# Kernel tuning notes

Hardware: AMD Instinct MI355X
Metric: run time of the kernel (lower is better)

## Reference

```python
import jax, jax.numpy as jnp
import numpy as np

BZ, MCN, HS, NC, LED, NT = 256, 128, 768, 7, 128, 2
EPS = 1e-12


def setup_inputs():
    key = jax.random.key(0)
    ks = jax.random.split(key, 16)
    def n(k, shape, sc=0.02):
        return jax.random.normal(k, shape, jnp.float32) * sc
    G4 = 4 * HS
    return {
        'clause_vector': jax.random.normal(ks[0], (BZ, MCN, HS), jnp.float32),
        'clause_num_mask': jnp.ones((BZ, MCN), jnp.float32),
        'target_labels': jax.random.uniform(ks[1], (BZ, MCN, NC), jnp.float32),
        'label_embed': n(ks[2], (NC, LED)),
        'Wq': n(ks[3], (HS, HS)), 'bq': jnp.zeros((HS,), jnp.float32),
        'Wk': n(ks[4], (HS, HS)), 'bk': jnp.zeros((HS,), jnp.float32),
        'Wv': n(ks[5], (HS, HS)), 'bv': jnp.zeros((HS,), jnp.float32),
        'Wo': n(ks[6], (HS, HS)), 'bo': jnp.zeros((HS,), jnp.float32),
        'ln_g': jnp.ones((HS,), jnp.float32), 'ln_b': jnp.zeros((HS,), jnp.float32),
        'Wp': n(ks[7], (HS, LED + 2 * HS)), 'bp': jnp.zeros((HS,), jnp.float32),
        'W_ih0': n(ks[8], (G4, HS)), 'W_hh0': n(ks[9], (G4, HS)),
        'b_ih0': jnp.zeros((G4,), jnp.float32), 'b_hh0': jnp.zeros((G4,), jnp.float32),
        'W_ih1': n(ks[10], (G4, HS)), 'W_hh1': n(ks[11], (G4, HS)),
        'b_ih1': jnp.zeros((G4,), jnp.float32), 'b_hh1': jnp.zeros((G4,), jnp.float32),
        'Wout': n(ks[12], (NC, HS)), 'bout': jnp.zeros((NC,), jnp.float32),
    }


def _layer_norm(x, g, b):
    mu = jnp.mean(x, -1, keepdims=True)
    var = jnp.mean(jnp.square(x - mu), -1, keepdims=True)
    return (x - mu) / jnp.sqrt(var + EPS) * g + b


def _forward(clause_vector, clause_num_mask, target_labels, label_embed,
             Wq, bq, Wk, bk, Wv, bv, Wo, bo, ln_g, ln_b, Wp, bp,
             W_ih0, W_hh0, b_ih0, b_hh0, W_ih1, W_hh1, b_ih1, b_hh1, Wout, bout):
    bz, mcn, hs = clause_vector.shape
    nc = Wout.shape[0]
    scale = float(1.0 / np.sqrt(hs))  # single head => head_size == hs
    # K/V depend only on clause_vector: hoist out of the decode loop
    K = clause_vector @ Wk.T + bk  # [bz, mcn, hs]
    V = clause_vector @ Wv.T + bv  # [bz, mcn, hs]
    mask_add = (1.0 - clause_num_mask) * -10000.0  # [bz, mcn]
    # step-0 labels: zeros with neutral (last) class set to 1 (remain_neutral)
    init_label = jnp.zeros((bz, nc), clause_vector.dtype).at[:, -1].set(1.0)
    # teacher forcing: step t>0 uses target_labels[:, t-1]
    lp_seq = jnp.concatenate([init_label[None], jnp.swapaxes(target_labels, 0, 1)[:-1]], 0)  # [mcn,bz,nc]
    cv_seq = jnp.swapaxes(clause_vector, 0, 1)  # [mcn, bz, hs]
    layers = ((W_ih0, W_hh0, b_ih0, b_hh0), (W_ih1, W_hh1, b_ih1, b_hh1))

    def step(carry, xs):
        h_all, c_all = carry  # [NT, bz, hs] each
        cv_t, lp = xs
        h = h_all[-1]  # decoder_hidden (dropout is identity in eval)
        emb = lp @ label_embed  # bmm(last_pred, label_embed) -> [bz, led]
        q = h @ Wq.T + bq
        scores = jnp.einsum('bh,bmh->bm', q, K) * scale + mask_add
        probs = jax.nn.softmax(scores, -1)
        ctx = jnp.einsum('bm,bmh->bh', probs, V)
        # BertSelfOutput: LayerNorm(dense(ctx) + residual)
        attn = _layer_norm(ctx @ Wo.T + bo + h, ln_g, ln_b)
        x = jnp.concatenate([emb, attn, cv_t], -1) @ Wp.T + bp  # [bz, hs]
        hs_new, cs_new = [], []
        for l, (Wih, Whh, bih, bhh) in enumerate(layers):
            gates = x @ Wih.T + bih + h_all[l] @ Whh.T + bhh  # [bz, 4hs]
            i, f, g, o = jnp.split(gates, 4, -1)  # torch gate order i,f,g,o
            c = jax.nn.sigmoid(f) * c_all[l] + jax.nn.sigmoid(i) * jnp.tanh(g)
            x = jax.nn.sigmoid(o) * jnp.tanh(c)
            hs_new.append(x)
            cs_new.append(c)
        h_all = jnp.stack(hs_new)
        c_all = jnp.stack(cs_new)
        pred = h_all[-1] @ Wout.T + bout  # raw logits (teacher-forcing branch)
        return (h_all, c_all), pred

    zeros = jnp.zeros((NT, bz, hs), clause_vector.dtype)
    _, preds = jax.lax.scan(step, (zeros, zeros), (cv_seq, lp_seq))
    return jnp.swapaxes(preds, 0, 1)  # [bz, mcn, nc]


def reference(clause_vector, clause_num_mask, target_labels, label_embed,
              Wq, bq, Wk, bk, Wv, bv, Wo, bo, ln_g, ln_b, Wp, bp,
              W_ih0, W_hh0, b_ih0, b_hh0, W_ih1, W_hh1, b_ih1, b_hh1, Wout, bout):
    return _forward(clause_vector, clause_num_mask, target_labels, label_embed,
                    Wq, bq, Wk, bk, Wv, bv, Wo, bo, ln_g, ln_b, Wp, bp,
                    W_ih0, W_hh0, b_ih0, b_hh0, W_ih1, W_hh1, b_ih1, b_hh1, Wout, bout)
```

## Files before the change

kernel.cpp:

```cpp
#include <hip/hip_runtime.h>
#include <hip/hip_bf16.h>
#include <math.h>

#define BZ 256
#define MCN 128
#define HS 768
#define NC 7
#define LED 128
#define G4 3072
#define LDP (LED + 2 * HS)

#define TBM 64
#define TBN 64
#define TBK 16

__device__ __forceinline__ ushort f2bf(float f) {
    uint x = __float_as_uint(f);
    uint r = (x + 0x7fffu + ((x >> 16) & 1u)) >> 16;
    return (ushort)r;
}
__device__ __forceinline__ float bf2f(ushort u) {
    return __uint_as_float(((uint)u) << 16);
}

__global__ __launch_bounds__(256) void gemm_abt(
    const float* __restrict__ A, int lda,
    const float* __restrict__ B, int ldb,
    const float* __restrict__ bias,
    const float* __restrict__ add, long add_ld,
    float* __restrict__ C, ushort* __restrict__ Cbf, int ldc, int K)
{
    __shared__ float As[TBK][TBM + 4];
    __shared__ float Bs[TBK][TBN + 4];
    const int tid = threadIdx.x;
    const int m0 = blockIdx.y * TBM;
    const int n0 = blockIdx.x * TBN;
    const int tx = tid & 15, ty = tid >> 4;
    const int lrow = tid >> 2;
    const int lcol = (tid & 3) * 4;
    float acc[4][4] = {};
    const float* Ap = A + (size_t)(m0 + lrow) * lda + lcol;
    const float* Bp = B + (size_t)(n0 + lrow) * ldb + lcol;
    for (int k0 = 0; k0 < K; k0 += TBK) {
        float4 av = *(const float4*)(Ap + k0);
        float4 bv = *(const float4*)(Bp + k0);
        As[lcol + 0][lrow] = av.x; As[lcol + 1][lrow] = av.y;
        As[lcol + 2][lrow] = av.z; As[lcol + 3][lrow] = av.w;
        Bs[lcol + 0][lrow] = bv.x; Bs[lcol + 1][lrow] = bv.y;
        Bs[lcol + 2][lrow] = bv.z; Bs[lcol + 3][lrow] = bv.w;
        __syncthreads();
        #pragma unroll
        for (int kk = 0; kk < TBK; ++kk) {
            float4 a4 = *(const float4*)&As[kk][ty * 4];
            float4 b4 = *(const float4*)&Bs[kk][tx * 4];
            float a[4] = {a4.x, a4.y, a4.z, a4.w};
            float b[4] = {b4.x, b4.y, b4.z, b4.w};
            #pragma unroll
            for (int i = 0; i < 4; ++i)
                #pragma unroll
                for (int j = 0; j < 4; ++j)
                    acc[i][j] += a[i] * b[j];
        }
        __syncthreads();
    }
    #pragma unroll
    for (int i = 0; i < 4; ++i) {
        int m = m0 + ty * 4 + i;
        #pragma unroll
        for (int j = 0; j < 4; ++j) {
            float v = acc[i][j];
            if (bias) v += bias[n0 + tx * 4 + j];
            if (add)  v += add[(size_t)m * add_ld + n0 + tx * 4 + j];
            if (Cbf) Cbf[(size_t)m * ldc + n0 + tx * 4 + j] = f2bf(v);
            else     C  [(size_t)m * ldc + n0 + tx * 4 + j] = v;
        }
    }
}

__global__ __launch_bounds__(256) void gemm_ab(
    const float* __restrict__ A, int lda,
    const float* __restrict__ B, int ldb,
    float* __restrict__ C, int ldc, int K)
{
    __shared__ float As[TBK][TBM + 4];
    __shared__ float Bs[TBK][TBN + 4];
    const int tid = threadIdx.x;
    const int m0 = blockIdx.y * TBM, n0 = blockIdx.x * TBN;
    const int tx = tid & 15, ty = tid >> 4;
    float acc[4][4] = {};
    for (int k0 = 0; k0 < K; k0 += TBK) {
        #pragma unroll
        for (int i = 0; i < 4; ++i) {
            int idx = tid + i * 256;
            int r = idx >> 4, kk = idx & 15;
            As[kk][r] = A[(size_t)(m0 + r) * lda + k0 + kk];
        }
        #pragma unroll
        for (int i = 0; i < 4; ++i) {
            int idx = tid + i * 256;
            int kk = idx >> 6, cc = idx & 63;
            Bs[kk][cc] = B[(size_t)(k0 + kk) * ldb + n0 + cc];
        }
        __syncthreads();
        #pragma unroll
        for (int kk = 0; kk < TBK; ++kk) {
            float4 a4 = *(const float4*)&As[kk][ty * 4];
            float4 b4 = *(const float4*)&Bs[kk][tx * 4];
            float a[4] = {a4.x, a4.y, a4.z, a4.w};
            float b[4] = {b4.x, b4.y, b4.z, b4.w};
            #pragma unroll
            for (int i = 0; i < 4; ++i)
                #pragma unroll
                for (int j = 0; j < 4; ++j)
                    acc[i][j] += a[i] * b[j];
        }
        __syncthreads();
    }
    #pragma unroll
    for (int i = 0; i < 4; ++i) {
        float* Cr = C + (size_t)(m0 + ty * 4 + i) * ldc + n0 + tx * 4;
        #pragma unroll
        for (int j = 0; j < 4; ++j) Cr[j] = acc[i][j];
    }
}

__global__ __launch_bounds__(256) void gemm_atb(
    const float* __restrict__ A, int lda,
    const float* __restrict__ B, int ldb,
    float* __restrict__ C, int ldc, int K, float alpha)
{
    __shared__ float As[TBK][TBM + 4];
    __shared__ float Bs[TBK][TBN + 4];
    const int tid = threadIdx.x;
    const int m0 = blockIdx.y * TBM, n0 = blockIdx.x * TBN;
    const int tx = tid & 15, ty = tid >> 4;
    float acc[4][4] = {};
    for (int k0 = 0; k0 < K; k0 += TBK) {
        #pragma unroll
        for (int i = 0; i < 4; ++i) {
            int idx = tid + i * 256;
            int kk = idx >> 6, r = idx & 63;
            As[kk][r] = A[(size_t)(k0 + kk) * lda + m0 + r];
            Bs[kk][r] = B[(size_t)(k0 + kk) * ldb + n0 + r];
        }
        __syncthreads();
        #pragma unroll
        for (int kk = 0; kk < TBK; ++kk) {
            float4 a4 = *(const float4*)&As[kk][ty * 4];
            float4 b4 = *(const float4*)&Bs[kk][tx * 4];
            float a[4] = {a4.x, a4.y, a4.z, a4.w};
            float b[4] = {b4.x, b4.y, b4.z, b4.w};
            #pragma unroll
            for (int i = 0; i < 4; ++i)
                #pragma unroll
                for (int j = 0; j < 4; ++j)
                    acc[i][j] += a[i] * b[j];
        }
        __syncthreads();
    }
    #pragma unroll
    for (int i = 0; i < 4; ++i) {
        float* Cr = C + (size_t)(m0 + ty * 4 + i) * ldc + n0 + tx * 4;
        #pragma unroll
        for (int j = 0; j < 4; ++j) Cr[j] = alpha * acc[i][j];
    }
}

__global__ __launch_bounds__(768) void attn_step(
    const float* __restrict__ h1, const ushort* __restrict__ Kp,
    const ushort* __restrict__ Vp, const float* __restrict__ cmask,
    const float* __restrict__ lng, const float* __restrict__ lnb,
    const float* __restrict__ bo,
    const float* __restrict__ Wout, const float* __restrict__ bout,
    float* __restrict__ out, float* __restrict__ attn_out, int t)
{
    __shared__ float hs[HS];
    __shared__ float sc[MCN];
    __shared__ float red[12];
    const int b = blockIdx.x, tid = threadIdx.x;
    const int lane = tid & 63, wv = tid >> 6;
    hs[tid] = h1[(size_t)b * HS + tid];
    __syncthreads();
    if (t > 0 && wv < NC) {
        const float* wr = Wout + (size_t)wv * HS;
        float s = 0.f;
        #pragma unroll
        for (int k = lane; k < HS; k += 64) s += hs[k] * wr[k];
        #pragma unroll
        for (int o = 32; o; o >>= 1) s += __shfl_down(s, o);
        if (lane == 0) out[((size_t)b * MCN + (t - 1)) * NC + wv] = s + bout[wv];
    }
    const ushort* Kb = Kp + (size_t)b * MCN * HS;
    for (int m = wv; m < MCN; m += 12) {
        const ushort* kr = Kb + (size_t)m * HS;
        float s = 0.f;
        #pragma unroll
        for (int k = lane * 2; k < HS; k += 128) {
            uint v = *(const uint*)(kr + k);
            s += hs[k] * bf2f((ushort)(v & 0xffffu))
               + hs[k + 1] * bf2f((ushort)(v >> 16));
        }
        #pragma unroll
        for (int o = 32; o; o >>= 1) s += __shfl_down(s, o);
        if (lane == 0) sc[m] = s + cmask[(size_t)b * MCN + m];
    }
    __syncthreads();
    if (tid < 64) {
        float a = sc[tid], c2 = sc[tid + 64];
        float mx = fmaxf(a, c2);
        #pragma unroll
        for (int o = 32; o; o >>= 1) mx = fmaxf(mx, __shfl_down(mx, o));
        mx = __shfl(mx, 0);
        float e0 = expf(a - mx), e1 = expf(c2 - mx);
        float ss = e0 + e1;
        #pragma unroll
        for (int o = 32; o; o >>= 1) ss += __shfl_down(ss, o);
        ss = __shfl(ss, 0);
        float inv = 1.0f / ss;
        sc[tid] = e0 * inv; sc[tid + 64] = e1 * inv;
    }
    __syncthreads();
    const int n = tid;
    const ushort* vp = Vp + (size_t)b * MCN * HS + n;
    float a = 0.f;
    #pragma unroll 8
    for (int m = 0; m < MCN; ++m) a += sc[m] * bf2f(vp[(size_t)m * HS]);
    a += bo[n] + hs[n];
    float lsum = a;
    #pragma unroll
    for (int o = 32; o; o >>= 1) lsum += __shfl_down(lsum, o);
    if (lane == 0) red[wv] = lsum;
    __syncthreads();
    float mu = 0.f;
    #pragma unroll
    for (int i = 0; i < 12; ++i) mu += red[i];
    mu *= (1.0f / HS);
    __syncthreads();
    float d = a - mu;
    float qq = d * d;
    #pragma unroll
    for (int o = 32; o; o >>= 1) qq += __shfl_down(qq, o);
    if (lane == 0) red[wv] = qq;
    __syncthreads();
    float var = 0.f;
    #pragma unroll
    for (int i = 0; i < 12; ++i) var += red[i];
    var *= (1.0f / HS);
    float inv = 1.0f / sqrtf(var + 1e-12f);
    attn_out[(size_t)b * HS + n] = d * inv * lng[n] + lnb[n];
}

__global__ __launch_bounds__(256) void lstm_step(
    const float* __restrict__ A1, const float* __restrict__ B1,
    const float* __restrict__ A2, const float* __restrict__ B2,
    const float* __restrict__ pre, size_t pre_stride,
    float* __restrict__ cbuf, float* __restrict__ hout)
{
    __shared__ float As[TBK][36];
    __shared__ float Bs[4][TBK][36];
    const int tid = threadIdx.x;
    const int n0 = blockIdx.x * 32;
    const int b0 = blockIdx.y * 32;
    const int rb = tid >> 5;
    const int nn = tid & 31;
    float acc[4][4] = {};
    #pragma unroll
    for (int ph = 0; ph < 2; ++ph) {
        const float* A = ph ? A2 : A1;
        const float* B = ph ? B2 : B1;
        for (int k0 = 0; k0 < HS; k0 += TBK) {
            #pragma unroll
            for (int i = 0; i < 2; ++i) {
                int idx = tid + i * 256;
                int r = idx >> 4, kk = idx & 15;
                As[kk][r] = A[(size_t)(b0 + r) * HS + k0 + kk];
            }
            #pragma unroll
            for (int i = 0; i < 8; ++i) {
                int idx = tid + i * 256;
                int s = idx >> 9, rem = idx & 511;
                int r = rem >> 4, kk = rem & 15;
                Bs[s][kk][r] = B[(size_t)(s * HS + n0 + r) * HS + k0 + kk];
            }
            __syncthreads();
            #pragma unroll
            for (int kk = 0; kk < TBK; ++kk) {
                float b0v = Bs[0][kk][nn], b1v = Bs[1][kk][nn];
                float b2v = Bs[2][kk][nn], b3v = Bs[3][kk][nn];
                #pragma unroll
                for (int k = 0; k < 4; ++k) {
                    float a = As[kk][rb + 8 * k];
                    acc[k][0] += a * b0v; acc[k][1] += a * b1v;
                    acc[k][2] += a * b2v; acc[k][3] += a * b3v;
                }
            }
            __syncthreads();
        }
    }
    #pragma unroll
    for (int k = 0; k < 4; ++k) {
        int b = b0 + rb + 8 * k;
        int n = n0 + nn;
        const float* pr = pre + (size_t)b * pre_stride;
        float ig = acc[k][0] + pr[n];
        float fg = acc[k][1] + pr[HS + n];
        float gg = acc[k][2] + pr[2 * HS + n];
        float og = acc[k][3] + pr[3 * HS + n];
        ig = 1.f / (1.f + expf(-ig));
        fg = 1.f / (1.f + expf(-fg));
        og = 1.f / (1.f + expf(-og));
        gg = tanhf(gg);
        size_t idx = (size_t)b * HS + n;
        float cn = fg * cbuf[idx] + ig * gg;
        cbuf[idx] = cn;
        hout[idx] = og * tanhf(cn);
    }
}

__global__ void bias_comb(const float* a, const float* b, const float* c, const float* d,
                          float* o0, float* o1)
{
    int i = blockIdx.x * blockDim.x + threadIdx.x;
    if (i < G4) { o0[i] = a[i] + b[i]; o1[i] = c[i] + d[i]; }
}

__global__ void t7_kernel(const float* __restrict__ LE, const float* __restrict__ Wp,
                          float* __restrict__ T7)
{
    int idx = blockIdx.x * blockDim.x + threadIdx.x;
    if (idx >= NC * HS) return;
    int c = idx / HS, n = idx % HS;
    float s = 0.f;
    for (int d = 0; d < LED; ++d) s += LE[c * LED + d] * Wp[(size_t)n * LDP + d];
    T7[idx] = s;
}

__global__ void fold_vecs(const float* __restrict__ Wq, const float* __restrict__ Wk,
                          const float* __restrict__ Wo,
                          const float* __restrict__ bq, const float* __restrict__ bk,
                          const float* __restrict__ bv,
                          float* __restrict__ bkq, float* __restrict__ bvo,
                          float* __restrict__ kqv, float scale)
{
    int j = blockIdx.x * 256 + threadIdx.x;
    if (j < HS) {
        float s1 = 0.f, s2 = 0.f, s3 = 0.f;
        for (int i = 0; i < HS; ++i) {
            s1 += bk[i] * Wq[(size_t)i * HS + j];
            s2 += bv[i] * Wo[(size_t)j * HS + i];
            s3 += bq[i] * Wk[(size_t)i * HS + j];
        }
        bkq[j] = s1 * scale; bvo[j] = s2; kqv[j] = s3 * scale;
    } else if (j == HS) {
        float s = 0.f;
        for (int i = 0; i < HS; ++i) s += bq[i] * bk[i];
        kqv[HS] = s * scale;
    }
}

__global__ __launch_bounds__(256) void cmask_kernel(
    const float* __restrict__ cv, const float* __restrict__ mask,
    const float* __restrict__ kqv, float* __restrict__ cm)
{
    int row = blockIdx.x * 4 + (threadIdx.x >> 6);
    int lane = threadIdx.x & 63;
    const float* r = cv + (size_t)row * HS;
    float s = 0.f;
    #pragma unroll
    for (int k = lane; k < HS; k += 64) s += r[k] * kqv[k];
    #pragma unroll
    for (int o = 32; o; o >>= 1) s += __shfl_down(s, o);
    if (lane == 0)
        cm[row] = s + kqv[HS] + (1.0f - mask[row]) * (-10000.0f);
}

__global__ void t7g_bp0(const float* __restrict__ T7, const float* __restrict__ Wih0,
                        const float* __restrict__ bp, const float* __restrict__ bih0,
                        const float* __restrict__ bhh0,
                        float* __restrict__ T7g, float* __restrict__ bp0)
{
    int g = blockIdx.x * 256 + threadIdx.x;
    if (g >= G4) return;
    float acc[NC] = {};
    float ab = 0.f;
    const float* wr = Wih0 + (size_t)g * HS;
    for (int n = 0; n < HS; ++n) {
        float w = wr[n];
        ab += bp[n] * w;
        #pragma unroll
        for (int c = 0; c < NC; ++c) acc[c] += T7[c * HS + n] * w;
    }
    #pragma unroll
    for (int c = 0; c < NC; ++c) T7g[c * G4 + g] = acc[c];
    bp0[g] = ab + bih0[g] + bhh0[g];
}

__global__ void gemb(float* __restrict__ gpre, const float* __restrict__ tl,
                     const float* __restrict__ T7g, const float* __restrict__ bp0)
{
    int g = blockIdx.x * 256 + threadIdx.x;
    size_t row = blockIdx.y;
    int t = (int)(row & (MCN - 1));
    float s = bp0[g];
    if (t == 0) s += T7g[(NC - 1) * G4 + g];
    else {
        const float* lp = tl + (row - 1) * NC;
        #pragma unroll
        for (int c = 0; c < NC; ++c) s += lp[c] * T7g[c * G4 + g];
    }
    gpre[row * G4 + g] += s;
}

__global__ void xemb_add(float* __restrict__ xpre, const float* __restrict__ tl,
                         const float* __restrict__ T7)
{
    int n = blockIdx.x * 256 + threadIdx.x;
    size_t row = blockIdx.y;
    int t = (int)(row & (MCN - 1));
    float s;
    if (t == 0) s = T7[(NC - 1) * HS + n];
    else {
        const float* lp = tl + (row - 1) * NC;
        s = 0.f;
        #pragma unroll
        for (int c = 0; c < NC; ++c) s += lp[c] * T7[c * HS + n];
    }
    xpre[row * HS + n] += s;
}

__global__ void emb_add(float* __restrict__ x, const float* __restrict__ tl,
                        const float* __restrict__ T7, int t)
{
    int n = blockIdx.x * 256 + threadIdx.x;
    int b = blockIdx.y;
    float s;
    if (t == 0) s = T7[(NC - 1) * HS + n];
    else {
        const float* lp = tl + ((size_t)b * MCN + (t - 1)) * NC;
        s = 0.f;
        #pragma unroll
        for (int c = 0; c < NC; ++c) s += lp[c] * T7[c * HS + n];
    }
    x[(size_t)b * HS + n] += s;
}

__global__ __launch_bounds__(64) void pred_kernel(
    const float* __restrict__ h1, const float* __restrict__ Wout,
    const float* __restrict__ bout, float* __restrict__ out, int t)
{
    const int b = blockIdx.x, c = blockIdx.y, lane = threadIdx.x;
    const float* hr = h1 + (size_t)b * HS;
    const float* wr = Wout + (size_t)c * HS;
    float s = 0.f;
    #pragma unroll
    for (int k = lane; k < HS; k += 64) s += hr[k] * wr[k];
    #pragma unroll
    for (int o = 32; o; o >>= 1) s += __shfl_down(s, o);
    if (lane == 0) out[((size_t)b * MCN + t) * NC + c] = s + bout[c];
}

extern "C" void kernel_launch(void* const* d_in, const int* in_sizes, int n_in,
                              void* d_out, int out_size, void* d_ws, size_t ws_size,
                              hipStream_t stream)
{
    (void)in_sizes; (void)n_in; (void)out_size;
    const float* cv   = (const float*)d_in[0];
    const float* mask = (const float*)d_in[1];
    const float* tl   = (const float*)d_in[2];
    const float* LE   = (const float*)d_in[3];
    const float* Wq   = (const float*)d_in[4];  const float* bq  = (const float*)d_in[5];
    const float* Wk   = (const float*)d_in[6];  const float* bk  = (const float*)d_in[7];
    const float* Wv   = (const float*)d_in[8];  const float* bv  = (const float*)d_in[9];
    const float* Wo   = (const float*)d_in[10]; const float* bo  = (const float*)d_in[11];
    const float* lng  = (const float*)d_in[12]; const float* lnb = (const float*)d_in[13];
    const float* Wp   = (const float*)d_in[14]; const float* bp  = (const float*)d_in[15];
    const float* Wih0 = (const float*)d_in[16]; const float* Whh0 = (const float*)d_in[17];
    const float* bih0 = (const float*)d_in[18]; const float* bhh0 = (const float*)d_in[19];
    const float* Wih1 = (const float*)d_in[20]; const float* Whh1 = (const float*)d_in[21];
    const float* bih1 = (const float*)d_in[22]; const float* bhh1 = (const float*)d_in[23];
    const float* Wout = (const float*)d_in[24]; const float* bout = (const float*)d_in[25];
    float* out = (float*)d_out;

    const size_t S_BH = (size_t)BZ * HS;
    const size_t S_KV = (size_t)BZ * MCN * HS;
    const size_t S_G  = (size_t)BZ * MCN * G4;

    float* w = (float*)d_ws;
    size_t off = 0;
    auto alloc = [&](size_t n) { off = (off + 3) & ~(size_t)3; float* p = w + off; off += n; return p; };
    ushort* Kbf  = (ushort*)alloc(S_KV / 2);
    ushort* Vbf  = (ushort*)alloc(S_KV / 2);
    float* cmask = alloc((size_t)BZ * MCN);
    float* attn  = alloc(S_BH);
    float* x     = alloc(S_BH);
    float* c0    = alloc(S_BH);
    float* c1    = alloc(S_BH);
    float* h0a   = alloc(S_BH);
    float* h1a   = alloc(S_BH);
    float* h0b   = alloc(S_BH);
    float* h1b   = alloc(S_BH);
    float* WkqT  = alloc((size_t)HS * HS);
    float* WvoT  = alloc((size_t)HS * HS);
    float* W0x   = alloc((size_t)G4 * HS);
    float* T7    = alloc((size_t)NC * HS);
    float* bc0   = alloc(G4);
    float* bc1   = alloc(G4);
    float* bkq   = alloc(HS);
    float* bvo   = alloc(HS);
    float* kqv   = alloc(HS + 1);
    off = (off + 3) & ~(size_t)3;
    const size_t base_end = off;
    float* W0c   = w + base_end;
    float* T7g   = W0c + (size_t)G4 * HS;
    float* bp0   = T7g + (size_t)NC * G4;
    float* gpre0 = bp0 + G4;
    const size_t full_end = (size_t)(gpre0 - w) + S_G;
    float* xpre  = w + base_end;
    const size_t A_end = base_end + S_KV;

    const int tier = (ws_size >= full_end * sizeof(float)) ? 2
                   : (ws_size >= A_end * sizeof(float))    ? 1 : 0;

    const float scale = 1.0f / sqrtf((float)HS);

    hipMemsetAsync(c0, 0, 4 * S_BH * sizeof(float), stream);
    bias_comb<<<(G4 + 255) / 256, 256, 0, stream>>>(bih0, bhh0, bih1, bhh1, bc0, bc1);
    t7_kernel<<<(NC * HS + 255) / 256, 256, 0, stream>>>(LE, Wp, T7);
    gemm_atb<<<dim3(12, 12), 256, 0, stream>>>(Wq, HS, Wk, HS, WkqT, HS, HS, scale);
    gemm_ab <<<dim3(12, 12), 256, 0, stream>>>(Wo, HS, Wv, HS, WvoT, HS, HS);
    gemm_ab <<<dim3(12, 48), 256, 0, stream>>>(Wih0, HS, Wp + LED, LDP, W0x, HS, HS);
    fold_vecs<<<4, 256, 0, stream>>>(Wq, Wk, Wo, bq, bk, bv, bkq, bvo, kqv, scale);
    cmask_kernel<<<(BZ * MCN) / 4, 256, 0, stream>>>(cv, mask, kqv, cmask);
    dim3 blk(256);
    gemm_abt<<<dim3(12, (BZ * MCN) / TBM), blk, 0, stream>>>(cv, HS, WkqT, HS, bkq, nullptr, 0,
                                                             nullptr, Kbf, HS, HS);
    gemm_abt<<<dim3(12, (BZ * MCN) / TBM), blk, 0, stream>>>(cv, HS, WvoT, HS, bvo, nullptr, 0,
                                                             nullptr, Vbf, HS, HS);
    if (tier == 2) {
        gemm_ab<<<dim3(12, 48), 256, 0, stream>>>(Wih0, HS, Wp + LED + HS, LDP, W0c, HS, HS);
        t7g_bp0<<<12, 256, 0, stream>>>(T7, Wih0, bp, bih0, bhh0, T7g, bp0);
        gemm_abt<<<dim3(48, (BZ * MCN) / TBM), blk, 0, stream>>>(cv, HS, W0c, HS, nullptr, nullptr, 0,
                                                                 gpre0, nullptr, G4, HS);
        gemb<<<dim3(12, BZ * MCN), 256, 0, stream>>>(gpre0, tl, T7g, bp0);
    } else if (tier == 1) {
        gemm_abt<<<dim3(12, (BZ * MCN) / TBM), blk, 0, stream>>>(cv, HS, Wp + LED + HS, LDP, bp,
                                                                 nullptr, 0, xpre, nullptr, HS, HS);
        xemb_add<<<dim3(3, BZ * MCN), 256, 0, stream>>>(xpre, tl, T7);
    }

    for (int t = 0; t < MCN; ++t) {
        const float* h0r = (t & 1) ? h0b : h0a;  float* h0w = (t & 1) ? h0a : h0b;
        const float* h1r = (t & 1) ? h1b : h1a;  float* h1w = (t & 1) ? h1a : h1b;
        attn_step<<<BZ, 768, 0, stream>>>(h1r, Kbf, Vbf, cmask, lng, lnb, bo,
                                          Wout, bout, out, attn, t);
        if (tier == 2) {
            lstm_step<<<dim3(24, 8), 256, 0, stream>>>(attn, W0x, h0r, Whh0,
                                                       gpre0 + (size_t)t * G4, (size_t)MCN * G4,
                                                       c0, h0w);
        } else {
            if (tier == 1) {
                gemm_abt<<<dim3(12, 4), blk, 0, stream>>>(attn, HS, Wp + LED, LDP, nullptr,
                                                          xpre + (size_t)t * HS, (size_t)MCN * HS,
                                                          x, nullptr, HS, HS);
            } else {
                gemm_abt<<<dim3(12, 4), blk, 0, stream>>>(attn, HS, Wp + LED, LDP, bp,
                                                          nullptr, 0, x, nullptr, HS, HS);
                gemm_abt<<<dim3(12, 4), blk, 0, stream>>>(cv + (size_t)t * HS, MCN * HS,
                                                          Wp + LED + HS, LDP, nullptr,
                                                          x, HS, x, nullptr, HS, HS);
                emb_add<<<dim3(3, BZ), 256, 0, stream>>>(x, tl, T7, t);
            }
            lstm_step<<<dim3(24, 8), 256, 0, stream>>>(x, Wih0, h0r, Whh0, bc0, 0, c0, h0w);
        }
        lstm_step<<<dim3(24, 8), 256, 0, stream>>>(h0w, Wih1, h1r, Whh1, bc1, 0, c1, h1w);
    }
    pred_kernel<<<dim3(BZ, NC), 64, 0, stream>>>(h1a, Wout, bout, out, MCN - 1);
}
```

Before: 44.14 ms.

## Fuse clause projection and label embedding into LSTM step with bf16 folded weights

Drops the precomputed gate pre-activation buffer (BZ*MCN*G4 floats), and with it the tier selection that depended on workspace size. The LSTM layer-0 kernel now runs three fused GEMM parts per step (attention output, the current clause vector, the hidden state) and adds the label-embedding term in its epilogue. The folded input weights are stored in bf16 and the LSTM kernel is double-buffered in shared memory. Per-step work grows by an extra K=768 part, trading that against the large precompute GEMM and its memory traffic, and bf16 weights lose some precision.

```diff
diff --git a/kernel.cpp b/kernel.cpp
--- a/kernel.cpp
+++ b/kernel.cpp
@@ -27,7 +27,6 @@
     const float* __restrict__ A, int lda,
     const float* __restrict__ B, int ldb,
     const float* __restrict__ bias,
-    const float* __restrict__ add, long add_ld,
     float* __restrict__ C, ushort* __restrict__ Cbf, int ldc, int K)
 {
     __shared__ float As[TBK][TBM + 4];
@@ -70,7 +69,6 @@
         for (int j = 0; j < 4; ++j) {
             float v = acc[i][j];
             if (bias) v += bias[n0 + tx * 4 + j];
-            if (add)  v += add[(size_t)m * add_ld + n0 + tx * 4 + j];
             if (Cbf) Cbf[(size_t)m * ldc + n0 + tx * 4 + j] = f2bf(v);
             else     C  [(size_t)m * ldc + n0 + tx * 4 + j] = v;
         }
@@ -80,7 +78,7 @@
 __global__ __launch_bounds__(256) void gemm_ab(
     const float* __restrict__ A, int lda,
     const float* __restrict__ B, int ldb,
-    float* __restrict__ C, int ldc, int K)
+    float* __restrict__ C, ushort* __restrict__ Cbf, int ldc, int K)
 {
     __shared__ float As[TBK][TBM + 4];
     __shared__ float Bs[TBK][TBN + 4];
@@ -118,9 +116,13 @@
     }
     #pragma unroll
     for (int i = 0; i < 4; ++i) {
-        float* Cr = C + (size_t)(m0 + ty * 4 + i) * ldc + n0 + tx * 4;
-        #pragma unroll
-        for (int j = 0; j < 4; ++j) Cr[j] = acc[i][j];
+        int m = m0 + ty * 4 + i;
+        #pragma unroll
+        for (int j = 0; j < 4; ++j) {
+            float v = acc[i][j];
+            if (Cbf) Cbf[(size_t)m * ldc + n0 + tx * 4 + j] = f2bf(v);
+            else     C  [(size_t)m * ldc + n0 + tx * 4 + j] = v;
+        }
     }
 }
 
@@ -250,66 +252,116 @@
     attn_out[(size_t)b * HS + n] = d * inv * lng[n] + lnb[n];
 }
 
-__global__ __launch_bounds__(256) void lstm_step(
-    const float* __restrict__ A1, const float* __restrict__ B1,
-    const float* __restrict__ A2, const float* __restrict__ B2,
-    const float* __restrict__ pre, size_t pre_stride,
+__global__ __launch_bounds__(256) void lstm_fused(
+    const float* __restrict__ A1, long s1, const void* __restrict__ B1, int f1,
+    const float* __restrict__ A2, long s2, const void* __restrict__ B2, int f2,
+    const float* __restrict__ A3, long s3, const void* __restrict__ B3, int f3,
+    int nparts,
+    const float* __restrict__ pre, const float* __restrict__ tl,
+    const float* __restrict__ T7g, int t,
     float* __restrict__ cbuf, float* __restrict__ hout)
 {
-    __shared__ float As[TBK][36];
-    __shared__ float Bs[4][TBK][36];
+    __shared__ float As[2][TBK][32];
+    __shared__ float Bs[2][TBK][32][4];
     const int tid = threadIdx.x;
     const int n0 = blockIdx.x * 32;
     const int b0 = blockIdx.y * 32;
-    const int rb = tid >> 5;
     const int nn = tid & 31;
+    const int mb = tid >> 5;
     float acc[4][4] = {};
-    #pragma unroll
-    for (int ph = 0; ph < 2; ++ph) {
-        const float* A = ph ? A2 : A1;
-        const float* B = ph ? B2 : B1;
-        for (int k0 = 0; k0 < HS; k0 += TBK) {
+
+    const int tiles_per_part = HS / TBK;
+    const int ntile = nparts * tiles_per_part;
+
+    auto stage = [&](int kt, int buf) {
+        int p = kt / tiles_per_part;
+        int k0 = (kt % tiles_per_part) * TBK;
+        const float* A; long as_; const void* B; int bf;
+        if (p == 0)      { A = A1; as_ = s1; B = B1; bf = f1; }
+        else if (p == 1) { A = A2; as_ = s2; B = B2; bf = f2; }
+        else             { A = A3; as_ = s3; B = B3; bf = f3; }
+        if (tid < 128) {
+            int r = tid >> 2, q = tid & 3;
+            float4 av = *(const float4*)(A + (long)(b0 + r) * as_ + k0 + q * 4);
+            As[buf][q * 4 + 0][r] = av.x; As[buf][q * 4 + 1][r] = av.y;
+            As[buf][q * 4 + 2][r] = av.z; As[buf][q * 4 + 3][r] = av.w;
+        }
+        #pragma unroll
+        for (int rep = 0; rep < 2; ++rep) {
+            int idx = tid + rep * 256;
+            int nn_ = idx & 31, s_ = (idx >> 5) & 3, q_ = idx >> 7;
+            long off = (long)(s_ * HS + n0 + nn_) * HS + k0 + q_ * 4;
+            float v0, v1, v2, v3;
+            if (bf) {
+                uint2 u = *(const uint2*)((const ushort*)B + off);
+                v0 = bf2f((ushort)(u.x & 0xffffu)); v1 = bf2f((ushort)(u.x >> 16));
+                v2 = bf2f((ushort)(u.y & 0xffffu)); v3 = bf2f((ushort)(u.y >> 16));
+            } else {
+                float4 bv = *(const float4*)((const float*)B + off);
+                v0 = bv.x; v1 = bv.y; v2 = bv.z; v3 = bv.w;
+            }
+            Bs[buf][q_ * 4 + 0][nn_][s_] = v0; Bs[buf][q_ * 4 + 1][nn_][s_] = v1;
+            Bs[buf][q_ * 4 + 2][nn_][s_] = v2; Bs[buf][q_ * 4 + 3][nn_][s_] = v3;
+        }
+    };
+
+    stage(0, 0);
+    int cur = 0;
+    for (int kt = 0; kt < ntile; ++kt) {
+        __syncthreads();
+        if (kt + 1 < ntile) stage(kt + 1, cur ^ 1);
+        #pragma unroll
+        for (int kk = 0; kk < TBK; ++kk) {
+            float4 a4 = *(const float4*)&As[cur][kk][mb * 4];
+            float4 b4 = *(const float4*)&Bs[cur][kk][nn][0];
+            float av[4] = {a4.x, a4.y, a4.z, a4.w};
+            float bv[4] = {b4.x, b4.y, b4.z, b4.w};
             #pragma unroll
-            for (int i = 0; i < 2; ++i) {
-                int idx = tid + i * 256;
-                int r = idx >> 4, kk = idx & 15;
-                As[kk][r] = A[(size_t)(b0 + r) * HS + k0 + kk];
-            }
+            for (int i = 0; i < 4; ++i)
+                #pragma unroll
+                for (int s = 0; s < 4; ++s)
+                    acc[i][s] += av[i] * bv[s];
+        }
+        cur ^= 1;
+    }
+
+    const int n = n0 + nn;
+    float pv[4];
+    #pragma unroll
+    for (int s = 0; s < 4; ++s) pv[s] = pre[s * HS + n];
+    float tg[NC][4];
+    if (tl) {
+        #pragma unroll
+        for (int c = 0; c < NC; ++c)
             #pragma unroll
-            for (int i = 0; i < 8; ++i) {
-                int idx = tid + i * 256;
-                int s = idx >> 9, rem = idx & 511;
-                int r = rem >> 4, kk = rem & 15;
-                Bs[s][kk][r] = B[(size_t)(s * HS + n0 + r) * HS + k0 + kk];
-            }
-            __syncthreads();
-            #pragma unroll
-            for (int kk = 0; kk < TBK; ++kk) {
-                float b0v = Bs[0][kk][nn], b1v = Bs[1][kk][nn];
-                float b2v = Bs[2][kk][nn], b3v = Bs[3][kk][nn];
+            for (int s = 0; s < 4; ++s)
+                tg[c][s] = T7g[(size_t)c * G4 + s * HS + n];
+    }
+    #pragma unroll
+    for (int i = 0; i < 4; ++i) {
+        int b = b0 + mb * 4 + i;
+        float g0 = acc[i][0] + pv[0];
+        float g1 = acc[i][1] + pv[1];
+        float g2 = acc[i][2] + pv[2];
+        float g3 = acc[i][3] + pv[3];
+        if (tl) {
+            if (t == 0) {
+                g0 += tg[NC - 1][0]; g1 += tg[NC - 1][1];
+                g2 += tg[NC - 1][2]; g3 += tg[NC - 1][3];
+            } else {
+                const float* lp = tl + ((size_t)b * MCN + (t - 1)) * NC;
                 #pragma unroll
-                for (int k = 0; k < 4; ++k) {
-                    float a = As[kk][rb + 8 * k];
-                    acc[k][0] += a * b0v; acc[k][1] += a * b1v;
-                    acc[k][2] += a * b2v; acc[k][3] += a * b3v;
+                for (int c = 0; c < NC; ++c) {
+                    float l = lp[c];
+                    g0 += l * tg[c][0]; g1 += l * tg[c][1];
+                    g2 += l * tg[c][2]; g3 += l * tg[c][3];
                 }
             }
-            __syncthreads();
-        }
-    }
-    #pragma unroll
-    for (int k = 0; k < 4; ++k) {
-        int b = b0 + rb + 8 * k;
-        int n = n0 + nn;
-        const float* pr = pre + (size_t)b * pre_stride;
-        float ig = acc[k][0] + pr[n];
-        float fg = acc[k][1] + pr[HS + n];
-        float gg = acc[k][2] + pr[2 * HS + n];
-        float og = acc[k][3] + pr[3 * HS + n];
-        ig = 1.f / (1.f + expf(-ig));
-        fg = 1.f / (1.f + expf(-fg));
-        og = 1.f / (1.f + expf(-og));
-        gg = tanhf(gg);
+        }
+        float ig = 1.f / (1.f + expf(-g0));
+        float fg = 1.f / (1.f + expf(-g1));
+        float gg = tanhf(g2);
+        float og = 1.f / (1.f + expf(-g3));
         size_t idx = (size_t)b * HS + n;
         float cn = fg * cbuf[idx] + ig * gg;
         cbuf[idx] = cn;
@@ -317,11 +369,10 @@
     }
 }
 
-__global__ void bias_comb(const float* a, const float* b, const float* c, const float* d,
-                          float* o0, float* o1)
-{
-    int i = blockIdx.x * blockDim.x + threadIdx.x;
-    if (i < G4) { o0[i] = a[i] + b[i]; o1[i] = c[i] + d[i]; }
+__global__ void vec_add2(const float* a, const float* b, float* o)
+{
+    int i = blockIdx.x * 256 + threadIdx.x;
+    if (i < G4) o[i] = a[i] + b[i];
 }
 
 __global__ void t7_kernel(const float* __restrict__ LE, const float* __restrict__ Wp,
@@ -391,57 +442,8 @@
         for (int c = 0; c < NC; ++c) acc[c] += T7[c * HS + n] * w;
     }
     #pragma unroll
-    for (int c = 0; c < NC; ++c) T7g[c * G4 + g] = acc[c];
+    for (int c = 0; c < NC; ++c) T7g[(size_t)c * G4 + g] = acc[c];
     bp0[g] = ab + bih0[g] + bhh0[g];
-}
-
-__global__ void gemb(float* __restrict__ gpre, const float* __restrict__ tl,
-                     const float* __restrict__ T7g, const float* __restrict__ bp0)
-{
-    int g = blockIdx.x * 256 + threadIdx.x;
-    size_t row = blockIdx.y;
-    int t = (int)(row & (MCN - 1));
-    float s = bp0[g];
-    if (t == 0) s += T7g[(NC - 1) * G4 + g];
-    else {
-        const float* lp = tl + (row - 1) * NC;
-        #pragma unroll
-        for (int c = 0; c < NC; ++c) s += lp[c] * T7g[c * G4 + g];
-    }
-    gpre[row * G4 + g] += s;
-}
-
-__global__ void xemb_add(float* __restrict__ xpre, const float* __restrict__ tl,
-                         const float* __restrict__ T7)
-{
-    int n = blockIdx.x * 256 + threadIdx.x;
-    size_t row = blockIdx.y;
-    int t = (int)(row & (MCN - 1));
-    float s;
-    if (t == 0) s = T7[(NC - 1) * HS + n];
-    else {
-        const float* lp = tl + (row - 1) * NC;
-        s = 0.f;
-        #pragma unroll
-        for (int c = 0; c < NC; ++c) s += lp[c] * T7[c * HS + n];
-    }
-    xpre[row * HS + n] += s;
-}
-
-__global__ void emb_add(float* __restrict__ x, const float* __restrict__ tl,
-                        const float* __restrict__ T7, int t)
-{
-    int n = blockIdx.x * 256 + threadIdx.x;
-    int b = blockIdx.y;
-    float s;
-    if (t == 0) s = T7[(NC - 1) * HS + n];
-    else {
-        const float* lp = tl + ((size_t)b * MCN + (t - 1)) * NC;
-        s = 0.f;
-        #pragma unroll
-        for (int c = 0; c < NC; ++c) s += lp[c] * T7[c * HS + n];
-    }
-    x[(size_t)b * HS + n] += s;
 }
 
 __global__ __launch_bounds__(64) void pred_kernel(
@@ -463,7 +465,7 @@
                               void* d_out, int out_size, void* d_ws, size_t ws_size,
                               hipStream_t stream)
 {
-    (void)in_sizes; (void)n_in; (void)out_size;
+    (void)in_sizes; (void)n_in; (void)out_size; (void)ws_size;
     const float* cv   = (const float*)d_in[0];
     const float* mask = (const float*)d_in[1];
     const float* tl   = (const float*)d_in[2];
@@ -483,96 +485,63 @@
 
     const size_t S_BH = (size_t)BZ * HS;
     const size_t S_KV = (size_t)BZ * MCN * HS;
-    const size_t S_G  = (size_t)BZ * MCN * G4;
 
     float* w = (float*)d_ws;
     size_t off = 0;
     auto alloc = [&](size_t n) { off = (off + 3) & ~(size_t)3; float* p = w + off; off += n; return p; };
-    ushort* Kbf  = (ushort*)alloc(S_KV / 2);
-    ushort* Vbf  = (ushort*)alloc(S_KV / 2);
-    float* cmask = alloc((size_t)BZ * MCN);
-    float* attn  = alloc(S_BH);
-    float* x     = alloc(S_BH);
-    float* c0    = alloc(S_BH);
-    float* c1    = alloc(S_BH);
-    float* h0a   = alloc(S_BH);
-    float* h1a   = alloc(S_BH);
-    float* h0b   = alloc(S_BH);
-    float* h1b   = alloc(S_BH);
-    float* WkqT  = alloc((size_t)HS * HS);
-    float* WvoT  = alloc((size_t)HS * HS);
-    float* W0x   = alloc((size_t)G4 * HS);
-    float* T7    = alloc((size_t)NC * HS);
-    float* bc0   = alloc(G4);
-    float* bc1   = alloc(G4);
-    float* bkq   = alloc(HS);
-    float* bvo   = alloc(HS);
-    float* kqv   = alloc(HS + 1);
-    off = (off + 3) & ~(size_t)3;
-    const size_t base_end = off;
-    float* W0c   = w + base_end;
-    float* T7g   = W0c + (size_t)G4 * HS;
-    float* bp0   = T7g + (size_t)NC * G4;
-    float* gpre0 = bp0 + G4;
-    const size_t full_end = (size_t)(gpre0 - w) + S_G;
-    float* xpre  = w + base_end;
-    const size_t A_end = base_end + S_KV;
-
-    const int tier = (ws_size >= full_end * sizeof(float)) ? 2
-                   : (ws_size >= A_end * sizeof(float))    ? 1 : 0;
+    ushort* Kbf   = (ushort*)alloc(S_KV / 2);
+    ushort* Vbf   = (ushort*)alloc(S_KV / 2);
+    float*  cmask = alloc((size_t)BZ * MCN);
+    ushort* W0xbf = (ushort*)alloc((size_t)G4 * HS / 2);
+    ushort* W0cbf = (ushort*)alloc((size_t)G4 * HS / 2);
+    float*  WkqT  = alloc((size_t)HS * HS);
+    float*  WvoT  = alloc((size_t)HS * HS);
+    float*  c1    = alloc(S_BH);
+    float*  T7    = alloc((size_t)NC * HS);
+    float*  T7g   = alloc((size_t)NC * G4);
+    float*  bp0   = alloc(G4);
+    float*  bc1   = alloc(G4);
+    float*  bkq   = alloc(HS);
+    float*  bvo   = alloc(HS);
+    float*  kqv   = alloc(HS + 1);
+    float* h1a  = WkqT;
+    float* h0a  = WkqT + S_BH;
+    float* attn = WkqT + 2 * S_BH;
+    float* h1b  = WvoT;
+    float* h0b  = WvoT + S_BH;
+    float* c0   = WvoT + 2 * S_BH;
 
     const float scale = 1.0f / sqrtf((float)HS);
-
-    hipMemsetAsync(c0, 0, 4 * S_BH * sizeof(float), stream);
-    bias_comb<<<(G4 + 255) / 256, 256, 0, stream>>>(bih0, bhh0, bih1, bhh1, bc0, bc1);
+    dim3 blk(256);
+
     t7_kernel<<<(NC * HS + 255) / 256, 256, 0, stream>>>(LE, Wp, T7);
-    gemm_atb<<<dim3(12, 12), 256, 0, stream>>>(Wq, HS, Wk, HS, WkqT, HS, HS, scale);
-    gemm_ab <<<dim3(12, 12), 256, 0, stream>>>(Wo, HS, Wv, HS, WvoT, HS, HS);
-    gemm_ab <<<dim3(12, 48), 256, 0, stream>>>(Wih0, HS, Wp + LED, LDP, W0x, HS, HS);
+    gemm_atb<<<dim3(12, 12), blk, 0, stream>>>(Wq, HS, Wk, HS, WkqT, HS, HS, scale);
+    gemm_ab <<<dim3(12, 12), blk, 0, stream>>>(Wo, HS, Wv, HS, WvoT, nullptr, HS, HS);
+    gemm_ab <<<dim3(12, 48), blk, 0, stream>>>(Wih0, HS, Wp + LED,      LDP, nullptr, W0xbf, HS, HS);
+    gemm_ab <<<dim3(12, 48), blk, 0, stream>>>(Wih0, HS, Wp + LED + HS, LDP, nullptr, W0cbf, HS, HS);
     fold_vecs<<<4, 256, 0, stream>>>(Wq, Wk, Wo, bq, bk, bv, bkq, bvo, kqv, scale);
     cmask_kernel<<<(BZ * MCN) / 4, 256, 0, stream>>>(cv, mask, kqv, cmask);
-    dim3 blk(256);
-    gemm_abt<<<dim3(12, (BZ * MCN) / TBM), blk, 0, stream>>>(cv, HS, WkqT, HS, bkq, nullptr, 0,
-                                                             nullptr, Kbf, HS, HS);
-    gemm_abt<<<dim3(12, (BZ * MCN) / TBM), blk, 0, stream>>>(cv, HS, WvoT, HS, bvo, nullptr, 0,
-                                                             nullptr, Vbf, HS, HS);
-    if (tier == 2) {
-        gemm_ab<<<dim3(12, 48), 256, 0, stream>>>(Wih0, HS, Wp + LED + HS, LDP, W0c, HS, HS);
-        t7g_bp0<<<12, 256, 0, stream>>>(T7, Wih0, bp, bih0, bhh0, T7g, bp0);
-        gemm_abt<<<dim3(48, (BZ * MCN) / TBM), blk, 0, stream>>>(cv, HS, W0c, HS, nullptr, nullptr, 0,
-                                                                 gpre0, nullptr, G4, HS);
-        gemb<<<dim3(12, BZ * MCN), 256, 0, stream>>>(gpre0, tl, T7g, bp0);
-    } else if (tier == 1) {
-        gemm_abt<<<dim3(12, (BZ * MCN) / TBM), blk, 0, stream>>>(cv, HS, Wp + LED + HS, LDP, bp,
-                                                                 nullptr, 0, xpre, nullptr, HS, HS);
-        xemb_add<<<dim3(3, BZ * MCN), 256, 0, stream>>>(xpre, tl, T7);
-    }
+    t7g_bp0<<<12, 256, 0, stream>>>(T7, Wih0, bp, bih0, bhh0, T7g, bp0);
+    vec_add2<<<12, 256, 0, stream>>>(bih1, bhh1, bc1);
+    gemm_abt<<<dim3(12, (BZ * MCN) / TBM), blk, 0, stream>>>(cv, HS, WkqT, HS, bkq, nullptr, Kbf, HS, HS);
+    gemm_abt<<<dim3(12, (BZ * MCN) / TBM), blk, 0, stream>>>(cv, HS, WvoT, HS, bvo, nullptr, Vbf, HS, HS);
+    hipMemsetAsync(WkqT, 0, 7 * S_BH * sizeof(float), stream);
 
     for (int t = 0; t < MCN; ++t) {
         const float* h0r = (t & 1) ? h0b : h0a;  float* h0w = (t & 1) ? h0a : h0b;
         const float* h1r = (t & 1) ? h1b : h1a;  float* h1w = (t & 1) ? h1a : h1b;
         attn_step<<<BZ, 768, 0, stream>>>(h1r, Kbf, Vbf, cmask, lng, lnb, bo,
                                           Wout, bout, out, attn, t);
-        if (tier == 2) {
-            lstm_step<<<dim3(24, 8), 256, 0, stream>>>(attn, W0x, h0r, Whh0,
-                                                       gpre0 + (size_t)t * G4, (size_t)MCN * G4,
-                                                       c0, h0w);
-        } else {
-            if (tier == 1) {
-                gemm_abt<<<dim3(12, 4), blk, 0, stream>>>(attn, HS, Wp + LED, LDP, nullptr,
-                                                          xpre + (size_t)t * HS, (size_t)MCN * HS,
-                                                          x, nullptr, HS, HS);
-            } else {
-                gemm_abt<<<dim3(12, 4), blk, 0, stream>>>(attn, HS, Wp + LED, LDP, bp,
-                                                          nullptr, 0, x, nullptr, HS, HS);
-                gemm_abt<<<dim3(12, 4), blk, 0, stream>>>(cv + (size_t)t * HS, MCN * HS,
-                                                          Wp + LED + HS, LDP, nullptr,
-                                                          x, HS, x, nullptr, HS, HS);
-                emb_add<<<dim3(3, BZ), 256, 0, stream>>>(x, tl, T7, t);
-            }
-            lstm_step<<<dim3(24, 8), 256, 0, stream>>>(x, Wih0, h0r, Whh0, bc0, 0, c0, h0w);
-        }
-        lstm_step<<<dim3(24, 8), 256, 0, stream>>>(h0w, Wih1, h1r, Whh1, bc1, 0, c1, h1w);
+        lstm_fused<<<dim3(24, 8), blk, 0, stream>>>(
+            attn, (long)HS, W0xbf, 1,
+            cv + (size_t)t * HS, (long)MCN * HS, W0cbf, 1,
+            h0r, (long)HS, Whh0, 0, 3,
+            bp0, tl, T7g, t, c0, h0w);
+        lstm_fused<<<dim3(24, 8), blk, 0, stream>>>(
+            h0w, (long)HS, Wih1, 0,
+            h1r, (long)HS, Whh1, 0,
+            nullptr, 0, nullptr, 0, 2,
+            bc1, nullptr, nullptr, 0, c1, h1w);
     }
     pred_kernel<<<dim3(BZ, NC), 64, 0, stream>>>(h1a, Wout, bout, out, MCN - 1);
 }
```

After: 47.80 ms. 8.3% more time.
